# Kernel optimization log

Hardware: AMD Instinct MI355X
Metric: run time of the kernel (lower is better)

The kernel has to match this reference:

```python
import jax, jax.numpy as jnp
import numpy as np

B, HID = 32768, 64


def setup_inputs() -> dict:
    key = jax.random.key(0)
    ks = jax.random.split(key, 16)
    N = 128
    inp = {
        "z": jax.random.normal(ks[0], (B, 2), jnp.float32),
        "u": jax.random.uniform(ks[1], (B, 2, N - 1), jnp.float32),
        "w0_1": jax.random.normal(ks[2], (HID, 1), jnp.float32) * 0.5,
        "b0_1": jax.random.normal(ks[3], (HID,), jnp.float32) * 0.1,
        "w0_2": jax.random.normal(ks[4], (HID, HID), jnp.float32) * (1.0 / np.sqrt(HID)),
        "b0_2": jax.random.normal(ks[5], (HID,), jnp.float32) * 0.1,
        "w0_3": jax.random.normal(ks[6], (1, HID), jnp.float32) * (1.0 / np.sqrt(HID)),
        "b0_3": jax.random.normal(ks[7], (1,), jnp.float32) * 0.1,
        "w1_1": jax.random.normal(ks[8], (HID, 1), jnp.float32) * 0.5,
        "b1_1": jax.random.normal(ks[9], (HID,), jnp.float32) * 0.1,
        "w1_2": jax.random.normal(ks[10], (HID, HID), jnp.float32) * (1.0 / np.sqrt(HID)),
        "b1_2": jax.random.normal(ks[11], (HID,), jnp.float32) * 0.1,
        "w1_3": jax.random.normal(ks[12], (1, HID), jnp.float32) * (1.0 / np.sqrt(HID)),
        "b1_3": jax.random.normal(ks[13], (1,), jnp.float32) * 0.1,
        "bias": jax.random.uniform(ks[14], (1,), jnp.float32),
        "N": N,
        "lower_bound": -5,
    }
    return inp


def _mlp(x, w1, b1, w2, b2, w3, b3):
    # x: (B, N) scalar inputs; 1 -> HID -> HID -> 1 with LeakyReLU(0.01), final ELU
    h = jax.nn.leaky_relu(x[..., None] * w1[:, 0] + b1, 0.01)          # (B, N, HID)
    h = jax.nn.leaky_relu(jnp.einsum("bnh,kh->bnk", h, w2) + b2, 0.01)  # (B, N, HID)
    o = jax.nn.elu(jnp.einsum("bnk,k->bn", h, w3[0]) + b3[0])           # (B, N)
    return o


def reference(z, u, w0_1, b0_1, w0_2, b0_2, w0_3, b0_3,
              w1_1, b1_1, w1_2, b1_2, w1_3, b1_3, bias, N, lower_bound):
    lb = jnp.asarray(lower_bound, z.dtype)
    zc = jnp.clip(z, lb, None)                         # clamp(min=lower_bound)
    d_size = (zc - lb) / jnp.asarray(N - 1, z.dtype)   # (B, 2)
    grid = jnp.arange(N, dtype=z.dtype)                # (N,)
    z_split = d_size[:, :, None] * grid + lb           # (B, 2, N)
    # jitter: U(0, d_size) for first N-1 bins, 0 for the last bin
    zeros_last = jnp.zeros(z_split.shape[:2] + (1,), z.dtype)
    z_random = z_split + jnp.concatenate([u * d_size[:, :, None], zeros_last], axis=-1)
    out0 = _mlp(z_random[:, 0, :], w0_1, b0_1, w0_2, b0_2, w0_3, b0_3)  # (B, N)
    out1 = _mlp(z_random[:, 1, :], w1_1, b1_1, w1_2, b1_2, w1_3, b1_3)  # (B, N)
    Hz0 = ((out0 + 1.0) * d_size[:, 0:1]).sum(axis=1)  # (B,)
    Hz1 = ((out1 + 1.0) * d_size[:, 1:2]).sum(axis=1)  # (B,)
    return Hz0 + Hz1 + bias[0]                         # (B,)
```

## Files before the change

kernel.cpp:

```cpp
#include <hip/hip_runtime.h>

#define NT 2048
#define XMAX 8.0f


__global__ __launch_bounds__(256) void build_table(
    const float* __restrict__ w01, const float* __restrict__ b01,
    const float* __restrict__ w02, const float* __restrict__ b02,
    const float* __restrict__ w03, const float* __restrict__ b03,
    const float* __restrict__ w11, const float* __restrict__ b11,
    const float* __restrict__ w12, const float* __restrict__ b12,
    const float* __restrict__ w13, const float* __restrict__ b13,
    const int* __restrict__ lbp, float* __restrict__ T)
{
    __shared__ float W2s[4096];
    __shared__ float w1s[64], b1s[64], b2s[64], w3s[64];

    const int tid = threadIdx.x;
    const int d  = blockIdx.x & 1;
    const int e0 = (blockIdx.x >> 1) * 64;

    const float* w1p = d ? w11 : w01;
    const float* b1p = d ? b11 : b01;
    const float* w2p = d ? w12 : w02;
    const float* b2p = d ? b12 : b02;
    const float* w3p = d ? w13 : w03;
    const float  b3  = (d ? b13 : b03)[0];

    #pragma unroll
    for (int j = 0; j < 16; ++j)
        W2s[tid + 256 * j] = w2p[tid + 256 * j];
    if (tid < 64) {
        w1s[tid] = w1p[tid];
        b1s[tid] = b1p[tid];
        b2s[tid] = b2p[tid];
        w3s[tid] = w3p[tid];
    }
    __syncthreads();

    const int e   = e0 + (tid >> 2);
    const int sub = tid & 3;

    const float lb = (float)lbp[0];
    const float delta = (XMAX - lb) / (float)(NT - 1);
    const float x = fmaf((float)e, delta, lb);

    float h1[64];
    #pragma unroll
    for (int k = 0; k < 64; ++k) {
        const float t = fmaf(x, w1s[k], b1s[k]);
        h1[k] = fmaxf(t, 0.01f * t);
    }

    float s = 0.0f;
    #pragma unroll 2
    for (int ff = 0; ff < 16; ++ff) {
        const int f = sub * 16 + ff;
        const float4* row = (const float4*)&W2s[f * 64];
        float a = b2s[f];
        #pragma unroll
        for (int k4 = 0; k4 < 16; ++k4) {
            const float4 w = row[k4];
            a = fmaf(w.x, h1[4 * k4 + 0], a);
            a = fmaf(w.y, h1[4 * k4 + 1], a);
            a = fmaf(w.z, h1[4 * k4 + 2], a);
            a = fmaf(w.w, h1[4 * k4 + 3], a);
        }
        s = fmaf(fmaxf(a, 0.01f * a), w3s[f], s);
    }

    s += __shfl_xor(s, 1);
    s += __shfl_xor(s, 2);
    if (sub == 0) T[d * NT + e] = s + b3;
}

__global__ __launch_bounds__(256) void integrate_tab(
    const float* __restrict__ zin, const float* __restrict__ uin,
    const float* __restrict__ Tg, const int* __restrict__ lbp,
    const float* __restrict__ biasp, float* __restrict__ out)
{
    __shared__ float Ts[2][NT];
    __shared__ float lds_hz[4][8];

    const int tid  = threadIdx.x;
    const int lane = tid & 63;
    const int wave = tid >> 6;
    const int d    = wave & 1;
    const int bg   = wave >> 1;
    const int b0 = blockIdx.x * 16 + bg * 8;

    const float lb = (float)lbp[0];
    const float scale = (float)(NT - 1) / (XMAX - lb);
    const float biasv = biasp[0];

    #pragma unroll
    for (int j = 0; j < 2 * NT / 256; ++j)
        ((float*)Ts)[tid + j * 256] = Tg[tid + j * 256];
    __syncthreads();

    const float* Td = Ts[d];
    const float n0 = (float)(2 * lane);
    const float n1 = (float)(2 * lane + 1);
    const bool last = (lane == 63);

    float z_n = zin[b0 * 2 + d];
    float2 u_n;
    {
        const float* ub = uin + (size_t)(b0 * 2 + d) * 127;
        u_n.x = ub[2 * lane];
        u_n.y = last ? 0.0f : ub[2 * lane + 1];
    }

    #pragma unroll 1
    for (int i = 0; i < 8; ++i) {
        const float zv = z_n;
        const float2 uu = u_n;

        const int bn = b0 + ((i < 7) ? i + 1 : 7);
        z_n = zin[bn * 2 + d];
        {
            const float* ub = uin + (size_t)(bn * 2 + d) * 127;
            u_n.x = ub[2 * lane];
            u_n.y = last ? 0.0f : ub[2 * lane + 1];
        }

        const float ds  = (fmaxf(zv, lb) - lb) * (1.0f / 127.0f);
        const float dsc = ds * scale;
        const float t0 = (n0 + uu.x) * dsc;
        const float t1 = (n1 + uu.y) * dsc;

        int i0 = (int)t0; i0 = min(i0, NT - 2);
        int i1 = (int)t1; i1 = min(i1, NT - 2);
        const float f0 = t0 - (float)i0;
        const float f1 = t1 - (float)i1;

        const float a0 = Td[i0], a0b = Td[i0 + 1];
        const float a1 = Td[i1], a1b = Td[i1 + 1];
        const float s0 = fmaf(f0, a0b - a0, a0);
        const float s1 = fmaf(f1, a1b - a1, a1);

        const float e0 = __builtin_amdgcn_exp2f(s0 * 1.4426950408889634f);
        const float e1 = __builtin_amdgcn_exp2f(s1 * 1.4426950408889634f);
        float acc = ((s0 > 0.0f) ? (s0 + 1.0f) : e0)
                  + ((s1 > 0.0f) ? (s1 + 1.0f) : e1);

        acc += __shfl_xor(acc, 1);
        acc += __shfl_xor(acc, 2);
        acc += __shfl_xor(acc, 4);
        acc += __shfl_xor(acc, 8);
        acc += __shfl_xor(acc, 16);
        acc += __shfl_xor(acc, 32);

        if (lane == 0) lds_hz[wave][i] = acc * ds;
    }

    __syncthreads();
    if (tid < 16) {
        const int g = tid >> 3, l = tid & 7;
        out[blockIdx.x * 16 + g * 8 + l] = lds_hz[2 * g][l] + lds_hz[2 * g + 1][l] + biasv;
    }
}

extern "C" void kernel_launch(void* const* d_in, const int* in_sizes, int n_in,
                              void* d_out, int out_size, void* d_ws, size_t ws_size,
                              hipStream_t stream) {
    const float* z    = (const float*)d_in[0];
    const float* u    = (const float*)d_in[1];
    const float* w0_1 = (const float*)d_in[2];
    const float* b0_1 = (const float*)d_in[3];
    const float* w0_2 = (const float*)d_in[4];
    const float* b0_2 = (const float*)d_in[5];
    const float* w0_3 = (const float*)d_in[6];
    const float* b0_3 = (const float*)d_in[7];
    const float* w1_1 = (const float*)d_in[8];
    const float* b1_1 = (const float*)d_in[9];
    const float* w1_2 = (const float*)d_in[10];
    const float* b1_2 = (const float*)d_in[11];
    const float* w1_3 = (const float*)d_in[12];
    const float* b1_3 = (const float*)d_in[13];
    const float* bias = (const float*)d_in[14];
    const int*   lbp  = (const int*)d_in[16];

    float* T = (float*)d_ws;

    build_table<<<dim3(64), dim3(256), 0, stream>>>(
        w0_1, b0_1, w0_2, b0_2, w0_3, b0_3,
        w1_1, b1_1, w1_2, b1_2, w1_3, b1_3,
        lbp, T);

    integrate_tab<<<dim3(2048), dim3(256), 0, stream>>>(z, u, T, lbp, bias, (float*)d_out);
}
```

Measured before the change: 120.9 us.

## Spread table build over more blocks, pad LDS rows, use DPP wave reduction

The table-building kernel now gives each table entry to 16 threads instead of 4, each handling 4 hidden features. It launches 256 blocks instead of 64, so more compute units share the table construction. The W2 rows in LDS are padded to a stride of 76 floats to reduce bank conflicts on the strided float4 reads. The integration kernel replaces its six-step xor-shuffle reduction with a DPP row_shr/row_bcast sequence that leaves the wave sum in lane 63, cutting the cost of cross-lane data movement. The trade-off is that the build step needs two extra shuffle steps and more blocks each reloading W2.

```diff
diff --git a/kernel.cpp b/kernel.cpp
--- a/kernel.cpp
+++ b/kernel.cpp
@@ -3,6 +3,22 @@
 #define NT 2048
 #define XMAX 8.0f
 
+
+__device__ __forceinline__ float wave_sum_lane63(float v) {
+#define DPP_ADD(ctrl)                                                         \
+    v += __int_as_float(__builtin_amdgcn_update_dpp(                          \
+        0, __float_as_int(v), (ctrl), 0xf, 0xf, false))
+    DPP_ADD(0x111);
+    DPP_ADD(0x112);
+    DPP_ADD(0x114);
+    DPP_ADD(0x118);
+    DPP_ADD(0x142);
+    DPP_ADD(0x143);
+#undef DPP_ADD
+    return v;
+}
+
+#define W2STRIDE 76
 
 __global__ __launch_bounds__(256) void build_table(
     const float* __restrict__ w01, const float* __restrict__ b01,
@@ -13,12 +29,12 @@
     const float* __restrict__ w13, const float* __restrict__ b13,
     const int* __restrict__ lbp, float* __restrict__ T)
 {
-    __shared__ float W2s[4096];
+    __shared__ float W2s[64 * W2STRIDE];
     __shared__ float w1s[64], b1s[64], b2s[64], w3s[64];
 
     const int tid = threadIdx.x;
     const int d  = blockIdx.x & 1;
-    const int e0 = (blockIdx.x >> 1) * 64;
+    const int e0 = (blockIdx.x >> 1) * 16;
 
     const float* w1p = d ? w11 : w01;
     const float* b1p = d ? b11 : b01;
@@ -28,8 +44,10 @@
     const float  b3  = (d ? b13 : b03)[0];
 
     #pragma unroll
-    for (int j = 0; j < 16; ++j)
-        W2s[tid + 256 * j] = w2p[tid + 256 * j];
+    for (int j = 0; j < 16; ++j) {
+        const int idx = tid + 256 * j;
+        W2s[(idx >> 6) * W2STRIDE + (idx & 63)] = w2p[idx];
+    }
     if (tid < 64) {
         w1s[tid] = w1p[tid];
         b1s[tid] = b1p[tid];
@@ -38,8 +56,8 @@
     }
     __syncthreads();
 
-    const int e   = e0 + (tid >> 2);
-    const int sub = tid & 3;
+    const int e   = e0 + (tid >> 4);
+    const int sub = tid & 15;
 
     const float lb = (float)lbp[0];
     const float delta = (XMAX - lb) / (float)(NT - 1);
@@ -53,10 +71,10 @@
     }
 
     float s = 0.0f;
-    #pragma unroll 2
-    for (int ff = 0; ff < 16; ++ff) {
-        const int f = sub * 16 + ff;
-        const float4* row = (const float4*)&W2s[f * 64];
+    #pragma unroll
+    for (int ff = 0; ff < 4; ++ff) {
+        const int f = (sub << 2) + ff;
+        const float4* row = (const float4*)&W2s[f * W2STRIDE];
         float a = b2s[f];
         #pragma unroll
         for (int k4 = 0; k4 < 16; ++k4) {
@@ -71,6 +89,8 @@
 
     s += __shfl_xor(s, 1);
     s += __shfl_xor(s, 2);
+    s += __shfl_xor(s, 4);
+    s += __shfl_xor(s, 8);
     if (sub == 0) T[d * NT + e] = s + b3;
 }
 
@@ -144,14 +164,9 @@
         float acc = ((s0 > 0.0f) ? (s0 + 1.0f) : e0)
                   + ((s1 > 0.0f) ? (s1 + 1.0f) : e1);
 
-        acc += __shfl_xor(acc, 1);
-        acc += __shfl_xor(acc, 2);
-        acc += __shfl_xor(acc, 4);
-        acc += __shfl_xor(acc, 8);
-        acc += __shfl_xor(acc, 16);
-        acc += __shfl_xor(acc, 32);
-
-        if (lane == 0) lds_hz[wave][i] = acc * ds;
+        acc = wave_sum_lane63(acc);
+
+        if (lane == 63) lds_hz[wave][i] = acc * ds;
     }
 
     __syncthreads();
@@ -183,7 +198,7 @@
 
     float* T = (float*)d_ws;
 
-    build_table<<<dim3(64), dim3(256), 0, stream>>>(
+    build_table<<<dim3(256), dim3(256), 0, stream>>>(
         w0_1, b0_1, w0_2, b0_2, w0_3, b0_3,
         w1_1, b1_1, w1_2, b1_2, w1_3, b1_3,
         lbp, T);
```

Result: faster. 112.6 us, median of 2 (-6.9%).
